# Performance work log

Measured on AMD Instinct MI355X. Metric: run time of the kernel, lower is better.

## Reference

```python
import jax, jax.numpy as jnp
import numpy as np

B = 8192      # molecules
L = 64        # atoms per molecule (equal-length segments)
D = 128       # atom_embed_dim
H = 4         # attention heads
FD = 64       # learned_feature_dim


def setup_inputs() -> dict:
    key = jax.random.key(0)
    ks = jax.random.split(key, 8)
    s = 0.02
    atom_embeddings = jax.random.normal(ks[0], (B * L, D), dtype=jnp.float32)
    batch_indices = jnp.repeat(jnp.arange(B, dtype=jnp.int64), L)
    # nn.MultiheadAttention in_proj: packed [3D, D] weight, [3D] bias (y = x @ W.T + b)
    W_in = jax.random.normal(ks[1], (3 * D, D), dtype=jnp.float32) * s
    b_in = jax.random.normal(ks[2], (3 * D,), dtype=jnp.float32) * s
    W_out = jax.random.normal(ks[3], (D, D), dtype=jnp.float32) * s
    b_out = jax.random.normal(ks[4], (D,), dtype=jnp.float32) * s
    # 4 pool projections, each Linear(D, FD//4)
    W_pool = jax.random.normal(ks[5], (4, FD // 4, D), dtype=jnp.float32) * s
    b_pool = jax.random.normal(ks[6], (4, FD // 4), dtype=jnp.float32) * s
    return {"atom_embeddings": atom_embeddings, "batch_indices": batch_indices,
            "W_in": W_in, "b_in": b_in, "W_out": W_out, "b_out": b_out,
            "W_pool": W_pool, "b_pool": b_pool}


def reference(atom_embeddings, batch_indices, W_in, b_in, W_out, b_out, W_pool, b_pool):
    # Equal-length segments: view as [B, L, D] batched molecules.
    x = atom_embeddings.reshape(B, L, D)
    dh = D // H

    # --- self-attention per molecule (eval mode: dropout off) ---
    qkv = jnp.einsum('bld,ed->ble', x, W_in) + b_in          # [B, L, 3D]
    q, k, v = jnp.split(qkv, 3, axis=-1)
    q = q.reshape(B, L, H, dh)
    k = k.reshape(B, L, H, dh)
    v = v.reshape(B, L, H, dh)
    scores = jnp.einsum('blhd,bmhd->bhlm', q, k) / np.sqrt(dh).astype(np.float32)
    probs = jax.nn.softmax(scores, axis=-1)
    ctx = jnp.einsum('bhlm,bmhd->blhd', probs, v).reshape(B, L, D)
    attended = jnp.einsum('bld,ed->ble', ctx, W_out) + b_out  # [B, L, D]

    # --- pooling ---
    aw = jax.nn.softmax(jnp.sum(attended * x, axis=-1), axis=-1)   # [B, L]
    weighted_mean = jnp.sum(attended * aw[..., None], axis=1)      # [B, D]
    max_pooled = jnp.max(attended, axis=1)
    mean_pooled = jnp.mean(attended, axis=1)
    std_pooled = jnp.std(attended, axis=1, ddof=1)                 # torch.std is unbiased
    pooled = jnp.stack([weighted_mean, max_pooled, mean_pooled, std_pooled], axis=1)  # [B, 4, D]

    # --- 4 small projections + concat ---
    proj = jnp.einsum('bpd,pfd->bpf', pooled, W_pool) + b_pool     # [B, 4, FD//4]
    return proj.reshape(B, FD)
```

## Files before the change

### kernel.cpp

```cpp
#include <hip/hip_runtime.h>
#include <hip/hip_bf16.h>

typedef short bf16x8 __attribute__((ext_vector_type(8)));
typedef float f32x4 __attribute__((ext_vector_type(4)));

struct __align__(8) us4 { unsigned short x, y, z, w; };

__device__ __forceinline__ unsigned short f2bfu(float f) {
  __hip_bfloat16 h = __float2bfloat16(f);
  unsigned short u; __builtin_memcpy(&u, &h, 2); return u;
}
__device__ __forceinline__ float bf2f(unsigned short u) {
  __hip_bfloat16 h; __builtin_memcpy(&h, &u, 2); return __bfloat162float(h);
}

constexpr int XB_STR  = 136;
constexpr int C_OFF   = 17408;
constexpr int QK_STR  = 264;
constexpr int P_STR   = 72;
constexpr int ATT_STR = 132;
constexpr int D_OFF   = 54272;
constexpr int VT_STR  = 72;
constexpr int CTX_STR = 136;
constexpr int F_OFF   = 72704;
constexpr int SMEM_BYTES = 79360;

__global__ void wconv_kernel(const float* __restrict__ win, const float* __restrict__ wout,
                             unsigned short* __restrict__ dst) {
  int i = blockIdx.x * 256 + threadIdx.x;
  float v = (i < 49152) ? win[i] : wout[i - 49152];
  dst[i] = f2bfu(v);
}

__global__ __launch_bounds__(256, 2)
void fused_mol_kernel(const float* __restrict__ xg_all,
                      const unsigned short* __restrict__ wb,
                      const float* __restrict__ b_in,
                      const float* __restrict__ b_out,
                      const float* __restrict__ W_pool,
                      const float* __restrict__ b_pool,
                      float* __restrict__ out)
{
  __shared__ __align__(16) char smem[SMEM_BYTES];
  const int tid  = threadIdx.x;
  const int wid  = tid >> 6;
  const int lane = tid & 63;
  const int lr   = lane & 15;
  const int lq   = lane >> 4;
  const int b    = blockIdx.x;

  unsigned short* xb  = (unsigned short*)(smem + 0);
  unsigned short* qk  = (unsigned short*)(smem + C_OFF);
  unsigned short* vt  = (unsigned short*)(smem + D_OFF);
  float* awlog  = (float*)(smem + F_OFF);
  float* aw     = (float*)(smem + F_OFF + 256);
  float* parts  = (float*)(smem + F_OFF + 512);
  float* pooled = (float*)(smem + F_OFF + 4608);

  const float* xg = xg_all + (long)b * (64 * 128);
  #pragma unroll
  for (int i = 0; i < 8; ++i) {
    int f = i * 1024 + tid * 4;
    const float4 v = *(const float4*)(xg + f);
    int row = f >> 7, col = f & 127;
    us4 h; h.x = f2bfu(v.x); h.y = f2bfu(v.y); h.z = f2bfu(v.z); h.w = f2bfu(v.w);
    *(us4*)(xb + row * XB_STR + col) = h;
  }
  __syncthreads();

  {
    const unsigned short* win = wb;
    bf16x8 Bf[6][4];
    #pragma unroll
    for (int nt = 0; nt < 6; ++nt) {
      int e = wid * 96 + nt * 16 + lr;
      #pragma unroll
      for (int k = 0; k < 4; ++k)
        Bf[nt][k] = *(const bf16x8*)(win + e * 128 + k * 32 + lq * 8);
    }
    #pragma unroll
    for (int mt = 0; mt < 4; ++mt) {
      bf16x8 Af[4];
      #pragma unroll
      for (int k = 0; k < 4; ++k)
        Af[k] = *(const bf16x8*)(xb + (mt * 16 + lr) * XB_STR + k * 32 + lq * 8);
      #pragma unroll
      for (int nt = 0; nt < 6; ++nt) {
        f32x4 acc = {0.f, 0.f, 0.f, 0.f};
        #pragma unroll
        for (int k = 0; k < 4; ++k)
          acc = __builtin_amdgcn_mfma_f32_16x16x32_bf16(Af[k], Bf[nt][k], acc, 0, 0, 0);
        int e = wid * 96 + nt * 16 + lr;
        float bias = b_in[e];
        int a0 = mt * 16 + lq * 4;
        if (e < 128) {
          const float sc = 0.17677669529663687f;
          #pragma unroll
          for (int r = 0; r < 4; ++r)
            qk[(a0 + r) * QK_STR + e] = f2bfu((acc[r] + bias) * sc);
        } else if (e < 256) {
          #pragma unroll
          for (int r = 0; r < 4; ++r)
            qk[(a0 + r) * QK_STR + e] = f2bfu(acc[r] + bias);
        } else {
          int dh = e - 256;
          us4 h;
          h.x = f2bfu(acc[0] + bias); h.y = f2bfu(acc[1] + bias);
          h.z = f2bfu(acc[2] + bias); h.w = f2bfu(acc[3] + bias);
          *(us4*)(vt + dh * VT_STR + a0) = h;
        }
      }
    }
  }
  __syncthreads();

  f32x4 sT[4][4];
  {
    f32x4 zero = {0.f, 0.f, 0.f, 0.f};
    bf16x8 Af[4], Bf2[4];
    #pragma unroll
    for (int mt = 0; mt < 4; ++mt)
      Af[mt] = *(const bf16x8*)(qk + (mt * 16 + lr) * QK_STR + 128 + wid * 32 + lq * 8);
    #pragma unroll
    for (int nt = 0; nt < 4; ++nt)
      Bf2[nt] = *(const bf16x8*)(qk + (nt * 16 + lr) * QK_STR + wid * 32 + lq * 8);
    #pragma unroll
    for (int mt = 0; mt < 4; ++mt)
      #pragma unroll
      for (int nt = 0; nt < 4; ++nt)
        sT[mt][nt] = __builtin_amdgcn_mfma_f32_16x16x32_bf16(Af[mt], Bf2[nt], zero, 0, 0, 0);
  }
  __syncthreads();

  unsigned short* pbuf = (unsigned short*)(smem + C_OFF) + wid * (64 * P_STR);
  #pragma unroll
  for (int nt = 0; nt < 4; ++nt) {
    float mx = -1e30f;
    #pragma unroll
    for (int mt = 0; mt < 4; ++mt)
      #pragma unroll
      for (int r = 0; r < 4; ++r) mx = fmaxf(mx, sT[mt][nt][r]);
    mx = fmaxf(mx, __shfl_xor(mx, 16));
    mx = fmaxf(mx, __shfl_xor(mx, 32));
    float ex[4][4]; float s = 0.f;
    #pragma unroll
    for (int mt = 0; mt < 4; ++mt)
      #pragma unroll
      for (int r = 0; r < 4; ++r) { ex[mt][r] = __expf(sT[mt][nt][r] - mx); s += ex[mt][r]; }
    s += __shfl_xor(s, 16);
    s += __shfl_xor(s, 32);
    float inv = 1.f / s;
    int l = nt * 16 + lr;
    #pragma unroll
    for (int mt = 0; mt < 4; ++mt) {
      us4 h;
      h.x = f2bfu(ex[mt][0] * inv); h.y = f2bfu(ex[mt][1] * inv);
      h.z = f2bfu(ex[mt][2] * inv); h.w = f2bfu(ex[mt][3] * inv);
      *(us4*)(pbuf + l * P_STR + mt * 16 + lq * 4) = h;
    }
  }

  f32x4 cacc[4][2];
  {
    #pragma unroll
    for (int mt = 0; mt < 4; ++mt)
      #pragma unroll
      for (int nt = 0; nt < 2; ++nt) cacc[mt][nt] = (f32x4){0.f, 0.f, 0.f, 0.f};
    #pragma unroll
    for (int kk = 0; kk < 2; ++kk) {
      bf16x8 Bf3[2];
      #pragma unroll
      for (int nt = 0; nt < 2; ++nt) {
        int dh = wid * 32 + nt * 16 + lr;
        Bf3[nt] = *(const bf16x8*)(vt + dh * VT_STR + kk * 32 + lq * 8);
      }
      #pragma unroll
      for (int mt = 0; mt < 4; ++mt) {
        bf16x8 Af = *(const bf16x8*)(pbuf + (mt * 16 + lr) * P_STR + kk * 32 + lq * 8);
        #pragma unroll
        for (int nt = 0; nt < 2; ++nt)
          cacc[mt][nt] = __builtin_amdgcn_mfma_f32_16x16x32_bf16(Af, Bf3[nt], cacc[mt][nt], 0, 0, 0);
      }
    }
  }
  __syncthreads();
  unsigned short* ctx = (unsigned short*)(smem + D_OFF);
  #pragma unroll
  for (int mt = 0; mt < 4; ++mt)
    #pragma unroll
    for (int nt = 0; nt < 2; ++nt) {
      int dhg = wid * 32 + nt * 16 + lr;
      int l0 = mt * 16 + lq * 4;
      #pragma unroll
      for (int r = 0; r < 4; ++r)
        ctx[(l0 + r) * CTX_STR + dhg] = f2bfu(cacc[mt][nt][r]);
    }
  __syncthreads();

  {
    const unsigned short* wout = wb + 49152;
    float* att = (float*)(smem + C_OFF);
    bf16x8 Bf4[2][4];
    #pragma unroll
    for (int nt = 0; nt < 2; ++nt) {
      int e = wid * 32 + nt * 16 + lr;
      #pragma unroll
      for (int k = 0; k < 4; ++k)
        Bf4[nt][k] = *(const bf16x8*)(wout + e * 128 + k * 32 + lq * 8);
    }
    #pragma unroll
    for (int mt = 0; mt < 4; ++mt) {
      bf16x8 Af[4];
      #pragma unroll
      for (int k = 0; k < 4; ++k)
        Af[k] = *(const bf16x8*)(ctx + (mt * 16 + lr) * CTX_STR + k * 32 + lq * 8);
      #pragma unroll
      for (int nt = 0; nt < 2; ++nt) {
        f32x4 acc = {0.f, 0.f, 0.f, 0.f};
        #pragma unroll
        for (int k = 0; k < 4; ++k)
          acc = __builtin_amdgcn_mfma_f32_16x16x32_bf16(Af[k], Bf4[nt][k], acc, 0, 0, 0);
        int e = wid * 32 + nt * 16 + lr;
        float bias = b_out[e];
        int l0 = mt * 16 + lq * 4;
        #pragma unroll
        for (int r = 0; r < 4; ++r)
          att[(l0 + r) * ATT_STR + e] = acc[r] + bias;
      }
    }
  }
  __syncthreads();

  float* att = (float*)(smem + C_OFF);
  {
    int l = tid >> 2, q = tid & 3;
    float s = 0.f;
    #pragma unroll
    for (int j = 0; j < 8; ++j) {
      int col = q * 32 + j * 4;
      float4 a = *(const float4*)(att + l * ATT_STR + col);
      us4 xh = *(const us4*)(xb + l * XB_STR + col);
      s += a.x * bf2f(xh.x) + a.y * bf2f(xh.y) + a.z * bf2f(xh.z) + a.w * bf2f(xh.w);
    }
    s += __shfl_xor(s, 1);
    s += __shfl_xor(s, 2);
    if (q == 0) awlog[l] = s;
  }
  __syncthreads();
  if (tid < 64) {
    float mx = -1e30f;
    for (int l = 0; l < 64; ++l) mx = fmaxf(mx, awlog[l]);
    float s = 0.f;
    for (int l = 0; l < 64; ++l) s += __expf(awlog[l] - mx);
    aw[tid] = __expf(awlog[tid] - mx) / s;
  }
  __syncthreads();
  {
    int e = tid & 127, hf = tid >> 7;
    float mx = -1e30f, s = 0.f, s2 = 0.f, ws = 0.f;
    for (int i = 0; i < 32; ++i) {
      int l = hf * 32 + i;
      float a = att[l * ATT_STR + e];
      float w = aw[l];
      mx = fmaxf(mx, a); s += a; s2 += a * a; ws += a * w;
    }
    float4 pr; pr.x = mx; pr.y = s; pr.z = s2; pr.w = ws;
    *(float4*)(parts + (hf * 128 + e) * 4) = pr;
  }
  __syncthreads();
  if (tid < 128) {
    int e = tid;
    float4 p0 = *(const float4*)(parts + e * 4);
    float4 p1 = *(const float4*)(parts + (128 + e) * 4);
    float mx = fmaxf(p0.x, p1.x);
    float s = p0.y + p1.y, s2 = p0.z + p1.z, ws = p0.w + p1.w;
    float mean = s * (1.f / 64.f);
    float var = (s2 - s * mean) * (1.f / 63.f);
    var = fmaxf(var, 0.f);
    pooled[0 * 128 + e] = ws;
    pooled[1 * 128 + e] = mx;
    pooled[2 * 128 + e] = mean;
    pooled[3 * 128 + e] = sqrtf(var);
  }
  __syncthreads();

  if (tid < 64) {
    int pp = tid >> 4;
    float acc = b_pool[tid];
    const float* wr = W_pool + tid * 128;
    #pragma unroll 8
    for (int d = 0; d < 128; d += 4) {
      float4 w = *(const float4*)(wr + d);
      float4 pl = *(const float4*)(pooled + pp * 128 + d);
      acc += w.x * pl.x + w.y * pl.y + w.z * pl.z + w.w * pl.w;
    }
    out[(long)b * 64 + tid] = acc;
  }
}

extern "C" void kernel_launch(void* const* d_in, const int* in_sizes, int n_in,
                              void* d_out, int out_size, void* d_ws, size_t ws_size,
                              hipStream_t stream) {
  const float* x      = (const float*)d_in[0];
  const float* W_in   = (const float*)d_in[2];
  const float* b_in   = (const float*)d_in[3];
  const float* W_out  = (const float*)d_in[4];
  const float* b_out  = (const float*)d_in[5];
  const float* W_pool = (const float*)d_in[6];
  const float* b_pool = (const float*)d_in[7];
  unsigned short* wb = (unsigned short*)d_ws;

  hipLaunchKernelGGL(wconv_kernel, dim3(256), dim3(256), 0, stream, W_in, W_out, wb);
  hipLaunchKernelGGL(fused_mol_kernel, dim3(8192), dim3(256), 0, stream,
                     x, wb, b_in, b_out, W_pool, b_pool, (float*)d_out);
}
```

Before: 558.4 us.

## Keep Q/K/V/P in registers, shrink LDS with swizzling, raise occupancy

Restructures the fused attention kernel so each wave computes its head's Q, K and V directly into registers and feeds them to the score and PV MFMAs without staging through shared memory. Shared memory drops from about 79KB to about 39KB by using XOR-swizzled bf16 layouts for x, ctx and the attended output, and launch bounds rise from 2 to 4 blocks per SM. Several barriers disappear, and the final softmax uses wave shuffles instead of a serial loop. In exchange the attended output is now held in bf16 rather than fp32, which costs some precision in pooling, and register pressure under the tighter launch bound may cause spills.

```diff
diff --git a/kernel.cpp b/kernel.cpp
--- a/kernel.cpp
+++ b/kernel.cpp
@@ -1,29 +1,34 @@
 #include <hip/hip_runtime.h>
 #include <hip/hip_bf16.h>
 
-typedef short bf16x8 __attribute__((ext_vector_type(8)));
-typedef float f32x4 __attribute__((ext_vector_type(4)));
-
-struct __align__(8) us4 { unsigned short x, y, z, w; };
+typedef short  bf16x8 __attribute__((ext_vector_type(8)));
+typedef float  f32x4  __attribute__((ext_vector_type(4)));
+typedef unsigned int u32;
+
+#define MFMA16(A,B,C) __builtin_amdgcn_mfma_f32_16x16x32_bf16((A),(B),(C),0,0,0)
 
 __device__ __forceinline__ unsigned short f2bfu(float f) {
   __hip_bfloat16 h = __float2bfloat16(f);
   unsigned short u; __builtin_memcpy(&u, &h, 2); return u;
 }
-__device__ __forceinline__ float bf2f(unsigned short u) {
-  __hip_bfloat16 h; __builtin_memcpy(&h, &u, 2); return __bfloat162float(h);
-}
-
-constexpr int XB_STR  = 136;
-constexpr int C_OFF   = 17408;
-constexpr int QK_STR  = 264;
-constexpr int P_STR   = 72;
-constexpr int ATT_STR = 132;
-constexpr int D_OFF   = 54272;
-constexpr int VT_STR  = 72;
-constexpr int CTX_STR = 136;
-constexpr int F_OFF   = 72704;
-constexpr int SMEM_BYTES = 79360;
+__device__ __forceinline__ u32 packbf(float lo, float hi) {
+  return (u32)f2bfu(lo) | ((u32)f2bfu(hi) << 16);
+}
+__device__ __forceinline__ float bfs(unsigned short u) {
+  return __uint_as_float(((u32)u) << 16);
+}
+__device__ __forceinline__ float bflo(u32 v) { return __uint_as_float(v << 16); }
+__device__ __forceinline__ float bfhi(u32 v) { return __uint_as_float(v & 0xffff0000u); }
+__device__ __forceinline__ bf16x8 mk8(u32 a, u32 b, u32 c, u32 d) {
+  union { bf16x8 h; u32 u[4]; } t; t.u[0] = a; t.u[1] = b; t.u[2] = c; t.u[3] = d; return t.h;
+}
+__device__ __forceinline__ int swz(int row, int colb) {
+  return row * 256 + (colb ^ ((row & 7) << 4));
+}
+
+constexpr int CTX_OFF = 16384;
+constexpr int F_OFF   = 32768;
+constexpr int SMEM_BYTES = 39424;
 
 __global__ void wconv_kernel(const float* __restrict__ win, const float* __restrict__ wout,
                              unsigned short* __restrict__ dst) {
@@ -32,7 +37,7 @@
   dst[i] = f2bfu(v);
 }
 
-__global__ __launch_bounds__(256, 2)
+__global__ __launch_bounds__(256, 4)
 void fused_mol_kernel(const float* __restrict__ xg_all,
                       const unsigned short* __restrict__ wb,
                       const float* __restrict__ b_in,
@@ -43,96 +48,91 @@
 {
   __shared__ __align__(16) char smem[SMEM_BYTES];
   const int tid  = threadIdx.x;
-  const int wid  = tid >> 6;
+  const int w    = tid >> 6;
   const int lane = tid & 63;
   const int lr   = lane & 15;
   const int lq   = lane >> 4;
-  const int b    = blockIdx.x;
-
-  unsigned short* xb  = (unsigned short*)(smem + 0);
-  unsigned short* qk  = (unsigned short*)(smem + C_OFF);
-  unsigned short* vt  = (unsigned short*)(smem + D_OFF);
+  const long b   = blockIdx.x;
+
+  char* xb = smem;
+  char* ca = smem + CTX_OFF;
   float* awlog  = (float*)(smem + F_OFF);
   float* aw     = (float*)(smem + F_OFF + 256);
   float* parts  = (float*)(smem + F_OFF + 512);
   float* pooled = (float*)(smem + F_OFF + 4608);
 
-  const float* xg = xg_all + (long)b * (64 * 128);
+  const float* xg = xg_all + b * (64 * 128);
   #pragma unroll
   for (int i = 0; i < 8; ++i) {
     int f = i * 1024 + tid * 4;
-    const float4 v = *(const float4*)(xg + f);
+    float4 v = *(const float4*)(xg + f);
     int row = f >> 7, col = f & 127;
-    us4 h; h.x = f2bfu(v.x); h.y = f2bfu(v.y); h.z = f2bfu(v.z); h.w = f2bfu(v.w);
-    *(us4*)(xb + row * XB_STR + col) = h;
-  }
-  __syncthreads();
-
-  {
-    const unsigned short* win = wb;
-    bf16x8 Bf[6][4];
-    #pragma unroll
-    for (int nt = 0; nt < 6; ++nt) {
-      int e = wid * 96 + nt * 16 + lr;
-      #pragma unroll
-      for (int k = 0; k < 4; ++k)
-        Bf[nt][k] = *(const bf16x8*)(win + e * 128 + k * 32 + lq * 8);
-    }
+    uint2 d; d.x = packbf(v.x, v.y); d.y = packbf(v.z, v.w);
+    *(uint2*)(xb + swz(row, col * 2)) = d;
+  }
+  __syncthreads();
+
+  u32 Qpk[2][4][2], Kpk[2][4][2];
+  {
+    f32x4 aq[2][4], ak[2][4];
+    #pragma unroll
+    for (int i = 0; i < 2; ++i)
+      #pragma unroll
+      for (int j = 0; j < 4; ++j) { aq[i][j] = (f32x4){0,0,0,0}; ak[i][j] = (f32x4){0,0,0,0}; }
+    #pragma unroll
+    for (int kk = 0; kk < 4; ++kk) {
+      bf16x8 Bx[4];
+      #pragma unroll
+      for (int j = 0; j < 4; ++j)
+        Bx[j] = *(const bf16x8*)(xb + swz(16 * j + lr, (kk * 32 + lq * 8) * 2));
+      bf16x8 Aq[2], Ak[2];
+      #pragma unroll
+      for (int i = 0; i < 2; ++i) {
+        Aq[i] = *(const bf16x8*)(wb + (w * 32 + 16 * i + lr) * 128 + kk * 32 + lq * 8);
+        Ak[i] = *(const bf16x8*)(wb + (128 + w * 32 + 16 * i + lr) * 128 + kk * 32 + lq * 8);
+      }
+      #pragma unroll
+      for (int i = 0; i < 2; ++i)
+        #pragma unroll
+        for (int j = 0; j < 4; ++j) {
+          aq[i][j] = MFMA16(Aq[i], Bx[j], aq[i][j]);
+          ak[i][j] = MFMA16(Ak[i], Bx[j], ak[i][j]);
+        }
+    }
+    const float sc = 0.17677669529663687f;
+    #pragma unroll
+    for (int i = 0; i < 2; ++i) {
+      float bq[4], bk[4];
+      #pragma unroll
+      for (int r = 0; r < 4; ++r) {
+        bq[r] = b_in[w * 32 + 16 * i + lq * 4 + r];
+        bk[r] = b_in[128 + w * 32 + 16 * i + lq * 4 + r];
+      }
+      #pragma unroll
+      for (int j = 0; j < 4; ++j) {
+        Qpk[i][j][0] = packbf((aq[i][j][0] + bq[0]) * sc, (aq[i][j][1] + bq[1]) * sc);
+        Qpk[i][j][1] = packbf((aq[i][j][2] + bq[2]) * sc, (aq[i][j][3] + bq[3]) * sc);
+        Kpk[i][j][0] = packbf(ak[i][j][0] + bk[0], ak[i][j][1] + bk[1]);
+        Kpk[i][j][1] = packbf(ak[i][j][2] + bk[2], ak[i][j][3] + bk[3]);
+      }
+    }
+  }
+
+  f32x4 sT[4][4];
+  {
+    const f32x4 z = (f32x4){0, 0, 0, 0};
     #pragma unroll
     for (int mt = 0; mt < 4; ++mt) {
-      bf16x8 Af[4];
-      #pragma unroll
-      for (int k = 0; k < 4; ++k)
-        Af[k] = *(const bf16x8*)(xb + (mt * 16 + lr) * XB_STR + k * 32 + lq * 8);
-      #pragma unroll
-      for (int nt = 0; nt < 6; ++nt) {
-        f32x4 acc = {0.f, 0.f, 0.f, 0.f};
-        #pragma unroll
-        for (int k = 0; k < 4; ++k)
-          acc = __builtin_amdgcn_mfma_f32_16x16x32_bf16(Af[k], Bf[nt][k], acc, 0, 0, 0);
-        int e = wid * 96 + nt * 16 + lr;
-        float bias = b_in[e];
-        int a0 = mt * 16 + lq * 4;
-        if (e < 128) {
-          const float sc = 0.17677669529663687f;
-          #pragma unroll
-          for (int r = 0; r < 4; ++r)
-            qk[(a0 + r) * QK_STR + e] = f2bfu((acc[r] + bias) * sc);
-        } else if (e < 256) {
-          #pragma unroll
-          for (int r = 0; r < 4; ++r)
-            qk[(a0 + r) * QK_STR + e] = f2bfu(acc[r] + bias);
-        } else {
-          int dh = e - 256;
-          us4 h;
-          h.x = f2bfu(acc[0] + bias); h.y = f2bfu(acc[1] + bias);
-          h.z = f2bfu(acc[2] + bias); h.w = f2bfu(acc[3] + bias);
-          *(us4*)(vt + dh * VT_STR + a0) = h;
-        }
-      }
-    }
-  }
-  __syncthreads();
-
-  f32x4 sT[4][4];
-  {
-    f32x4 zero = {0.f, 0.f, 0.f, 0.f};
-    bf16x8 Af[4], Bf2[4];
-    #pragma unroll
-    for (int mt = 0; mt < 4; ++mt)
-      Af[mt] = *(const bf16x8*)(qk + (mt * 16 + lr) * QK_STR + 128 + wid * 32 + lq * 8);
-    #pragma unroll
-    for (int nt = 0; nt < 4; ++nt)
-      Bf2[nt] = *(const bf16x8*)(qk + (nt * 16 + lr) * QK_STR + wid * 32 + lq * 8);
-    #pragma unroll
-    for (int mt = 0; mt < 4; ++mt)
-      #pragma unroll
-      for (int nt = 0; nt < 4; ++nt)
-        sT[mt][nt] = __builtin_amdgcn_mfma_f32_16x16x32_bf16(Af[mt], Bf2[nt], zero, 0, 0, 0);
-  }
-  __syncthreads();
-
-  unsigned short* pbuf = (unsigned short*)(smem + C_OFF) + wid * (64 * P_STR);
+      bf16x8 Ka = mk8(Kpk[0][mt][0], Kpk[0][mt][1], Kpk[1][mt][0], Kpk[1][mt][1]);
+      #pragma unroll
+      for (int nt = 0; nt < 4; ++nt) {
+        bf16x8 Qb = mk8(Qpk[0][nt][0], Qpk[0][nt][1], Qpk[1][nt][0], Qpk[1][nt][1]);
+        sT[mt][nt] = MFMA16(Ka, Qb, z);
+      }
+    }
+  }
+
+  u32 Ppk[4][4][2];
   #pragma unroll
   for (int nt = 0; nt < 4; ++nt) {
     float mx = -1e30f;
@@ -150,97 +150,112 @@
     s += __shfl_xor(s, 16);
     s += __shfl_xor(s, 32);
     float inv = 1.f / s;
-    int l = nt * 16 + lr;
     #pragma unroll
     for (int mt = 0; mt < 4; ++mt) {
-      us4 h;
-      h.x = f2bfu(ex[mt][0] * inv); h.y = f2bfu(ex[mt][1] * inv);
-      h.z = f2bfu(ex[mt][2] * inv); h.w = f2bfu(ex[mt][3] * inv);
-      *(us4*)(pbuf + l * P_STR + mt * 16 + lq * 4) = h;
-    }
-  }
-
-  f32x4 cacc[4][2];
-  {
-    #pragma unroll
-    for (int mt = 0; mt < 4; ++mt)
-      #pragma unroll
-      for (int nt = 0; nt < 2; ++nt) cacc[mt][nt] = (f32x4){0.f, 0.f, 0.f, 0.f};
+      Ppk[mt][nt][0] = packbf(ex[mt][0] * inv, ex[mt][1] * inv);
+      Ppk[mt][nt][1] = packbf(ex[mt][2] * inv, ex[mt][3] * inv);
+    }
+  }
+
+  u32 Vpk[4][2][2];
+  {
+    f32x4 av[4][2];
+    #pragma unroll
+    for (int m = 0; m < 4; ++m)
+      #pragma unroll
+      for (int j = 0; j < 2; ++j) av[m][j] = (f32x4){0, 0, 0, 0};
+    #pragma unroll
+    for (int kk = 0; kk < 4; ++kk) {
+      bf16x8 Ax[4];
+      #pragma unroll
+      for (int m = 0; m < 4; ++m)
+        Ax[m] = *(const bf16x8*)(xb + swz(16 * m + lr, (kk * 32 + lq * 8) * 2));
+      bf16x8 Bw[2];
+      #pragma unroll
+      for (int j = 0; j < 2; ++j)
+        Bw[j] = *(const bf16x8*)(wb + (256 + w * 32 + 16 * j + lr) * 128 + kk * 32 + lq * 8);
+      #pragma unroll
+      for (int m = 0; m < 4; ++m)
+        #pragma unroll
+        for (int j = 0; j < 2; ++j) av[m][j] = MFMA16(Ax[m], Bw[j], av[m][j]);
+    }
+    #pragma unroll
+    for (int j = 0; j < 2; ++j) {
+      float bv = b_in[256 + w * 32 + 16 * j + lr];
+      #pragma unroll
+      for (int m = 0; m < 4; ++m) {
+        Vpk[m][j][0] = packbf(av[m][j][0] + bv, av[m][j][1] + bv);
+        Vpk[m][j][1] = packbf(av[m][j][2] + bv, av[m][j][3] + bv);
+      }
+    }
+  }
+
+  {
+    f32x4 cacc[4][2];
+    #pragma unroll
+    for (int nt = 0; nt < 4; ++nt)
+      #pragma unroll
+      for (int j = 0; j < 2; ++j) cacc[nt][j] = (f32x4){0, 0, 0, 0};
     #pragma unroll
     for (int kk = 0; kk < 2; ++kk) {
-      bf16x8 Bf3[2];
-      #pragma unroll
-      for (int nt = 0; nt < 2; ++nt) {
-        int dh = wid * 32 + nt * 16 + lr;
-        Bf3[nt] = *(const bf16x8*)(vt + dh * VT_STR + kk * 32 + lq * 8);
-      }
-      #pragma unroll
-      for (int mt = 0; mt < 4; ++mt) {
-        bf16x8 Af = *(const bf16x8*)(pbuf + (mt * 16 + lr) * P_STR + kk * 32 + lq * 8);
+      #pragma unroll
+      for (int nt = 0; nt < 4; ++nt) {
+        bf16x8 Pa = mk8(Ppk[2 * kk][nt][0], Ppk[2 * kk][nt][1],
+                        Ppk[2 * kk + 1][nt][0], Ppk[2 * kk + 1][nt][1]);
         #pragma unroll
-        for (int nt = 0; nt < 2; ++nt)
-          cacc[mt][nt] = __builtin_amdgcn_mfma_f32_16x16x32_bf16(Af, Bf3[nt], cacc[mt][nt], 0, 0, 0);
-      }
-    }
-  }
-  __syncthreads();
-  unsigned short* ctx = (unsigned short*)(smem + D_OFF);
-  #pragma unroll
-  for (int mt = 0; mt < 4; ++mt)
-    #pragma unroll
-    for (int nt = 0; nt < 2; ++nt) {
-      int dhg = wid * 32 + nt * 16 + lr;
-      int l0 = mt * 16 + lq * 4;
-      #pragma unroll
-      for (int r = 0; r < 4; ++r)
-        ctx[(l0 + r) * CTX_STR + dhg] = f2bfu(cacc[mt][nt][r]);
-    }
-  __syncthreads();
-
-  {
-    const unsigned short* wout = wb + 49152;
-    float* att = (float*)(smem + C_OFF);
-    bf16x8 Bf4[2][4];
-    #pragma unroll
-    for (int nt = 0; nt < 2; ++nt) {
-      int e = wid * 32 + nt * 16 + lr;
-      #pragma unroll
-      for (int k = 0; k < 4; ++k)
-        Bf4[nt][k] = *(const bf16x8*)(wout + e * 128 + k * 32 + lq * 8);
-    }
-    #pragma unroll
-    for (int mt = 0; mt < 4; ++mt) {
-      bf16x8 Af[4];
-      #pragma unroll
-      for (int k = 0; k < 4; ++k)
-        Af[k] = *(const bf16x8*)(ctx + (mt * 16 + lr) * CTX_STR + k * 32 + lq * 8);
-      #pragma unroll
-      for (int nt = 0; nt < 2; ++nt) {
-        f32x4 acc = {0.f, 0.f, 0.f, 0.f};
-        #pragma unroll
-        for (int k = 0; k < 4; ++k)
-          acc = __builtin_amdgcn_mfma_f32_16x16x32_bf16(Af[k], Bf4[nt][k], acc, 0, 0, 0);
-        int e = wid * 32 + nt * 16 + lr;
-        float bias = b_out[e];
-        int l0 = mt * 16 + lq * 4;
+        for (int j = 0; j < 2; ++j) {
+          bf16x8 Vb = mk8(Vpk[2 * kk][j][0], Vpk[2 * kk][j][1],
+                          Vpk[2 * kk + 1][j][0], Vpk[2 * kk + 1][j][1]);
+          cacc[nt][j] = MFMA16(Pa, Vb, cacc[nt][j]);
+        }
+      }
+    }
+    #pragma unroll
+    for (int nt = 0; nt < 4; ++nt)
+      #pragma unroll
+      for (int j = 0; j < 2; ++j) {
+        int dhg = w * 32 + 16 * j + lr;
         #pragma unroll
         for (int r = 0; r < 4; ++r)
-          att[(l0 + r) * ATT_STR + e] = acc[r] + bias;
-      }
-    }
-  }
-  __syncthreads();
-
-  float* att = (float*)(smem + C_OFF);
+          *(unsigned short*)(ca + swz(16 * nt + lq * 4 + r, dhg * 2)) = f2bfu(cacc[nt][j][r]);
+      }
+  }
+  __syncthreads();
+
+  {
+    bf16x8 Actx[4];
+    #pragma unroll
+    for (int kk = 0; kk < 4; ++kk)
+      Actx[kk] = *(const bf16x8*)(ca + swz(16 * w + lr, (kk * 32 + lq * 8) * 2));
+    const unsigned short* wout = wb + 49152;
+    #pragma unroll
+    for (int nt = 0; nt < 8; ++nt) {
+      bf16x8 Bw[4];
+      #pragma unroll
+      for (int kk = 0; kk < 4; ++kk)
+        Bw[kk] = *(const bf16x8*)(wout + (16 * nt + lr) * 128 + kk * 32 + lq * 8);
+      f32x4 a = (f32x4){0, 0, 0, 0};
+      #pragma unroll
+      for (int kk = 0; kk < 4; ++kk) a = MFMA16(Actx[kk], Bw[kk], a);
+      float bo = b_out[16 * nt + lr];
+      int e = 16 * nt + lr;
+      #pragma unroll
+      for (int r = 0; r < 4; ++r)
+        *(unsigned short*)(ca + swz(16 * w + lq * 4 + r, e * 2)) = f2bfu(a[r] + bo);
+    }
+  }
+  __syncthreads();
+
   {
     int l = tid >> 2, q = tid & 3;
     float s = 0.f;
     #pragma unroll
-    for (int j = 0; j < 8; ++j) {
-      int col = q * 32 + j * 4;
-      float4 a = *(const float4*)(att + l * ATT_STR + col);
-      us4 xh = *(const us4*)(xb + l * XB_STR + col);
-      s += a.x * bf2f(xh.x) + a.y * bf2f(xh.y) + a.z * bf2f(xh.z) + a.w * bf2f(xh.w);
+    for (int jj = 0; jj < 8; ++jj) {
+      int colb = (q * 32 + jj * 4) * 2;
+      uint2 av = *(const uint2*)(ca + swz(l, colb));
+      uint2 xv = *(const uint2*)(xb + swz(l, colb));
+      s += bflo(av.x) * bflo(xv.x) + bfhi(av.x) * bfhi(xv.x)
+         + bflo(av.y) * bflo(xv.y) + bfhi(av.y) * bfhi(xv.y);
     }
     s += __shfl_xor(s, 1);
     s += __shfl_xor(s, 2);
@@ -248,11 +263,15 @@
   }
   __syncthreads();
   if (tid < 64) {
-    float mx = -1e30f;
-    for (int l = 0; l < 64; ++l) mx = fmaxf(mx, awlog[l]);
-    float s = 0.f;
-    for (int l = 0; l < 64; ++l) s += __expf(awlog[l] - mx);
-    aw[tid] = __expf(awlog[tid] - mx) / s;
+    float v = awlog[tid];
+    float mx = v;
+    #pragma unroll
+    for (int o = 1; o < 64; o <<= 1) mx = fmaxf(mx, __shfl_xor(mx, o));
+    float e = __expf(v - mx);
+    float s = e;
+    #pragma unroll
+    for (int o = 1; o < 64; o <<= 1) s += __shfl_xor(s, o);
+    aw[tid] = e / s;
   }
   __syncthreads();
   {
@@ -260,9 +279,9 @@
     float mx = -1e30f, s = 0.f, s2 = 0.f, ws = 0.f;
     for (int i = 0; i < 32; ++i) {
       int l = hf * 32 + i;
-      float a = att[l * ATT_STR + e];
-      float w = aw[l];
-      mx = fmaxf(mx, a); s += a; s2 += a * a; ws += a * w;
+      float a = bfs(*(const unsigned short*)(ca + swz(l, e * 2)));
+      float wgt = aw[l];
+      mx = fmaxf(mx, a); s += a; s2 += a * a; ws += a * wgt;
     }
     float4 pr; pr.x = mx; pr.y = s; pr.z = s2; pr.w = ws;
     *(float4*)(parts + (hf * 128 + e) * 4) = pr;
@@ -290,11 +309,11 @@
     const float* wr = W_pool + tid * 128;
     #pragma unroll 8
     for (int d = 0; d < 128; d += 4) {
-      float4 w = *(const float4*)(wr + d);
+      float4 wv = *(const float4*)(wr + d);
       float4 pl = *(const float4*)(pooled + pp * 128 + d);
-      acc += w.x * pl.x + w.y * pl.y + w.z * pl.z + w.w * pl.w;
-    }
-    out[(long)b * 64 + tid] = acc;
+      acc += wv.x * pl.x + wv.y * pl.y + wv.z * pl.z + wv.w * pl.w;
+    }
+    out[b * 64 + tid] = acc;
   }
 }
 
```

Measured after the change: 749.3 us. 34.2% more time.
